# Kernel tuning notes

Measured on AMD Instinct MI355X. Metric: run time of the kernel, lower is better.

Reference implementation:

```python
import jax, jax.numpy as jnp
import numpy as np

B, H, W, C = 2, 128, 128, 256
WS = 8            # current_window (query window)
KW = 16           # halo_window = 2*current_window
HEADS = 8
HD = C // HEADS
PRETRAIN = 8
CPB_HIDDEN = 512


def _rel_bias_consts():
    halo = (KW - WS) // 2
    coords = np.arange(1 - WS - halo, WS + halo, dtype=np.float32)  # length WS+KW-1 = 23
    tab = np.stack(np.meshgrid(coords, coords, indexing='ij'), axis=-1)  # [23,23,2]
    tab = tab * (8.0 / (PRETRAIN - 1.0))
    tab = np.sign(tab) * np.log1p(np.abs(tab)) / np.log(8.0)
    tab = tab.reshape(-1, 2).astype(np.float32)                      # [529,2]
    qi = np.arange(WS)
    qg = np.stack(np.meshgrid(qi, qi, indexing='ij')).reshape(2, -1)  # [2,64]
    ki = np.arange(KW)
    kg = np.stack(np.meshgrid(ki, ki, indexing='ij')).reshape(2, -1)  # [2,256]
    rel = qg[:, :, None] - kg[:, None] + (KW - 1)
    idx = (rel[0] * (WS + KW - 1) + rel[1]).reshape(-1).astype(np.int32)  # [64*256]
    return tab, idx

_REL_TAB, _REL_IDX = _rel_bias_consts()


def setup_inputs() -> dict:
    key = jax.random.key(0)
    ks = jax.random.split(key, 12)
    s = 0.02
    return {
        'x': jax.random.normal(ks[0], (B, H, W, C), jnp.float32),
        'w_qkv': jax.random.normal(ks[1], (C, 3 * C), jnp.float32) * s,
        'w_dw': jax.random.normal(ks[2], (3, 3, 1, 3 * C), jnp.float32) * s,  # depthwise HWIO
        'ln_g': jnp.ones((3 * C,), jnp.float32),
        'ln_b': jnp.zeros((3 * C,), jnp.float32),
        'q_bias': jnp.zeros((C,), jnp.float32),
        'v_bias': jnp.zeros((C,), jnp.float32),
        'logit_scale': jnp.full((HEADS, 1, 1), np.log(10.0), jnp.float32),
        'cpb_w1': jax.random.normal(ks[3], (2, CPB_HIDDEN), jnp.float32) * s,
        'cpb_b1': jnp.zeros((CPB_HIDDEN,), jnp.float32),
        'cpb_w2': jax.random.normal(ks[4], (CPB_HIDDEN, HEADS), jnp.float32) * s,
        'w_proj': jax.random.normal(ks[5], (C, C), jnp.float32) * s,
    }


def _l2n(t):
    # tf.math.l2_normalize with epsilon=1.55e-5
    return t * jax.lax.rsqrt(jnp.maximum(jnp.sum(t * t, -1, keepdims=True), 1.55e-5))


def reference(x, w_qkv, w_dw, ln_g, ln_b, q_bias, v_bias, logit_scale,
              cpb_w1, cpb_b1, cpb_w2, w_proj):
    nWh, nWw = H // WS, W // WS
    nW = nWh * nWw
    # qkv 1x1 conv + depthwise 3x3 + layernorm + (q,0,v) bias
    qkv = jnp.einsum('bhwc,cd->bhwd', x, w_qkv)
    qkv = jax.lax.conv_general_dilated(
        qkv, w_dw, (1, 1), 'SAME',
        dimension_numbers=('NHWC', 'HWIO', 'NHWC'), feature_group_count=3 * C)
    mu = jnp.mean(qkv, -1, keepdims=True)
    var = jnp.var(qkv, -1, keepdims=True)
    qkv = (qkv - mu) * jax.lax.rsqrt(var + 1e-5) * ln_g + ln_b
    qkv = qkv + jnp.concatenate([q_bias, jnp.zeros_like(q_bias), v_bias])
    q, kv = qkv[..., :C], qkv[..., C:]
    # window partition of q: [B*nW, heads, WS*WS, HD]
    qp = q.reshape(B, nWh, WS, nWw, WS, HEADS, HD)
    qp = qp.transpose(0, 1, 3, 5, 2, 4, 6).reshape(B * nW, HEADS, WS * WS, HD)
    # halo partition of kv: overlapping KWxKW patches, stride WS
    halo = (KW - WS) // 2
    kvp = jnp.pad(kv, ((0, 0), (halo, halo), (halo, halo), (0, 0)))
    ridx = (np.arange(nWh) * WS)[:, None] + np.arange(KW)[None]  # [nWh,KW]
    cidx = (np.arange(nWw) * WS)[:, None] + np.arange(KW)[None]  # [nWw,KW]
    kvp = kvp[:, ridx][:, :, :, cidx]               # [B,nWh,KW,nWw,KW,2C]
    kvp = kvp.transpose(0, 1, 3, 2, 4, 5).reshape(B * nW, KW * KW, 2, HEADS, HD)
    k = kvp[:, :, 0].transpose(0, 2, 1, 3)          # [B*nW, heads, KW*KW, HD]
    v = kvp[:, :, 1].transpose(0, 2, 1, 3)
    # cosine attention with clamped learned log-scale
    scale = jnp.exp(jnp.minimum(logit_scale, np.float32(np.log(100.0))))
    attn = jnp.einsum('whqd,whkd->whqk', _l2n(qp) * scale, _l2n(k))
    # continuous relative position bias (CPB MLP + gather)
    hidden = jax.nn.relu(jnp.asarray(_REL_TAB) @ cpb_w1 + cpb_b1)
    bias_tab = jax.nn.sigmoid(hidden @ cpb_w2) * 16.0        # [529, heads]
    rb = bias_tab[_REL_IDX].reshape(WS * WS, KW * KW, HEADS).transpose(2, 0, 1)
    attn = jax.nn.softmax(attn + rb[None], axis=-1)
    out = jnp.einsum('whqk,whkd->whqd', attn, v)             # [B*nW, heads, 64, HD]
    # reverse window partition
    out = out.reshape(B, nWh, nWw, HEADS, WS, WS, HD)
    out = out.transpose(0, 1, 4, 2, 5, 3, 6).reshape(B, H, W, C)
    return jnp.einsum('bhwc,cd->bhwd', out, w_proj)
```

## Files before the change

kernel.cpp:

```cpp
#include <hip/hip_runtime.h>
#include <hip/hip_bf16.h>
#include <hip/hip_fp16.h>
#include <cstddef>
#include <cstdint>

#define BB 2
#define HH 128
#define WW 128
#define CC 256
#define WSZ 8
#define KWIN 16
#define NHEADS 8
#define HD 32
#define C3 768
#define NPIX 32768
#define NWIN 512

typedef short    bf16x8 __attribute__((ext_vector_type(8)));
typedef _Float16 half8  __attribute__((ext_vector_type(8)));
typedef _Float16 half4v __attribute__((ext_vector_type(4)));
typedef float    f32x4  __attribute__((ext_vector_type(4)));

__device__ inline short f2bf(float f) {
    union { float f; unsigned u; } v; v.f = f;
    unsigned r = (v.u + 0x7fffu + ((v.u >> 16) & 1u)) >> 16;
    return (short)r;
}

__device__ inline void gload_lds16(const _Float16* g, _Float16* l) {
    __builtin_amdgcn_global_load_lds(
        (const __attribute__((address_space(1))) unsigned int*)g,
        (__attribute__((address_space(3))) unsigned int*)l, 16, 0, 0);
}

__global__ __launch_bounds__(64) void cpb_kernel(const float* __restrict__ w1,
                                                 const float* __restrict__ b1,
                                                 const float* __restrict__ w2,
                                                 float* __restrict__ btab) {
    const int e = blockIdx.x;
    const int i = e / 23, j = e % 23;
    const float inv_log8 = 1.0f / logf(8.0f);
    float c0 = (float)(i - 11) * (8.0f / 7.0f);
    float c1 = (float)(j - 11) * (8.0f / 7.0f);
    float f0 = copysignf(log1pf(fabsf(c0)) * inv_log8, c0);
    float f1 = copysignf(log1pf(fabsf(c1)) * inv_log8, c1);

    const int t = threadIdx.x;
    float acc[8] = {0.f,0.f,0.f,0.f,0.f,0.f,0.f,0.f};
    for (int kk = 0; kk < 8; kk++) {
        int k = kk * 64 + t;
        float hid = f0 * w1[k] + f1 * w1[512 + k] + b1[k];
        hid = fmaxf(hid, 0.f);
        #pragma unroll
        for (int h = 0; h < 8; h++) acc[h] += hid * w2[k * 8 + h];
    }
    #pragma unroll
    for (int h = 0; h < 8; h++) {
        #pragma unroll
        for (int off = 32; off >= 1; off >>= 1) acc[h] += __shfl_xor(acc[h], off);
    }
    if (t < 8) {
        float v = acc[t];
        btab[e * 8 + t] = 16.0f / (1.0f + expf(-v));
    }
}

__global__ __launch_bounds__(256) void cvt_f32_f16(const float* __restrict__ src,
                                                   _Float16* __restrict__ dst,
                                                   int n4) {
    int i = blockIdx.x * 256 + threadIdx.x;
    if (i >= n4) return;
    float4 v = *(const float4*)(src + (size_t)i * 4);
    half4v o; o[0] = (_Float16)v.x; o[1] = (_Float16)v.y;
    o[2] = (_Float16)v.z; o[3] = (_Float16)v.w;
    *(half4v*)(dst + (size_t)i * 4) = o;
}

__global__ __launch_bounds__(256) void transpose_cvt(const float* __restrict__ src,
                                                     _Float16* __restrict__ dst,
                                                     int R, int Cn) {
    __shared__ float t[32][33];
    const int bx = blockIdx.x, by = blockIdx.y;
    const int tx = threadIdx.x & 31, ty = threadIdx.x >> 5;
    #pragma unroll
    for (int i = 0; i < 4; i++) {
        int r = by * 32 + ty + i * 8;
        t[ty + i * 8][tx] = src[(size_t)r * Cn + bx * 32 + tx];
    }
    __syncthreads();
    #pragma unroll
    for (int i = 0; i < 4; i++) {
        int dr = bx * 32 + ty + i * 8;
        dst[(size_t)dr * R + by * 32 + tx] = (_Float16)t[tx][ty + i * 8];
    }
}

template <typename OT>
__global__ __launch_bounds__(256) void gemm_f16(const _Float16* __restrict__ A,
                                                const _Float16* __restrict__ Bt,
                                                OT* __restrict__ C,
                                                int M, int N, int K) {
    __shared__ _Float16 Ash[128][64];
    __shared__ _Float16 Bsh[128][64];
    const int tid = threadIdx.x;
    const int wv = tid >> 6, ln = tid & 63;
    const int quad = ln >> 4, l15 = ln & 15;
    const int rowb = blockIdx.y * 128;
    const int colb = blockIdx.x * 128;
    const int wm = (wv >> 1) * 64, wn = (wv & 1) * 64;

    const int r8 = ln >> 3, g = ln & 7;
    const int kg = g ^ r8;

    f32x4 acc[4][4] = {};
    for (int k0 = 0; k0 < K; k0 += 64) {
        #pragma unroll
        for (int i = 0; i < 4; i++) {
            const int m = wv * 32 + i * 8 + r8;
            gload_lds16(A + (size_t)(rowb + m) * K + k0 + kg * 8,
                        &Ash[wv * 32 + i * 8][0]);
            gload_lds16(Bt + (size_t)(colb + m) * K + k0 + kg * 8,
                        &Bsh[wv * 32 + i * 8][0]);
        }
        __syncthreads();
        #pragma unroll
        for (int kk = 0; kk < 2; kk++) {
            const int phys = ((kk * 4 + quad) ^ (l15 & 7)) * 8;
            half8 a[4], b[4];
            #pragma unroll
            for (int i = 0; i < 4; i++)
                a[i] = *(const half8*)&Ash[wm + i * 16 + l15][phys];
            #pragma unroll
            for (int j = 0; j < 4; j++)
                b[j] = *(const half8*)&Bsh[wn + j * 16 + l15][phys];
            #pragma unroll
            for (int i = 0; i < 4; i++)
                #pragma unroll
                for (int j = 0; j < 4; j++)
                    acc[i][j] = __builtin_amdgcn_mfma_f32_16x16x32_f16(
                        a[i], b[j], acc[i][j], 0, 0, 0);
        }
        __syncthreads();
    }
    #pragma unroll
    for (int i = 0; i < 4; i++) {
        #pragma unroll
        for (int reg = 0; reg < 4; reg++) {
            const size_t row = rowb + wm + i * 16 + quad * 4 + reg;
            #pragma unroll
            for (int j = 0; j < 4; j++) {
                C[row * N + colb + wn + j * 16 + l15] = (OT)acc[i][j][reg];
            }
        }
    }
}

__global__ __launch_bounds__(256) void dwconv_ln(const _Float16* __restrict__ in,
                                                 const float* __restrict__ wdw,
                                                 const float* __restrict__ g,
                                                 const float* __restrict__ bt,
                                                 const float* __restrict__ qb,
                                                 const float* __restrict__ vb,
                                                 _Float16* __restrict__ out) {
    __shared__ _Float16 S[3 * 10 * C3];
    __shared__ _Float16 Wl[9 * C3];
    __shared__ float sred[4][8][2];

    const int t = threadIdx.x;
    const int pix0 = blockIdx.x * 8;
    const int b = pix0 >> 14, y = (pix0 >> 7) & 127, x0 = pix0 & 127;

    for (int u = t; u < 864; u += 256) {
        const float4 w0 = *(const float4*)(wdw + u * 8);
        const float4 w1 = *(const float4*)(wdw + u * 8 + 4);
        half8 w;
        w[0] = (_Float16)w0.x; w[1] = (_Float16)w0.y;
        w[2] = (_Float16)w0.z; w[3] = (_Float16)w0.w;
        w[4] = (_Float16)w1.x; w[5] = (_Float16)w1.y;
        w[6] = (_Float16)w1.z; w[7] = (_Float16)w1.w;
        *(half8*)&Wl[u * 8] = w;
    }
    for (int u = t; u < 2880; u += 256) {
        const int r = u / 960, rem = u - r * 960;
        const int c = rem / 96, grp = rem - c * 96;
        const int yy = y + r - 1, xx = x0 + c - 1;
        half8 v = (half8)(_Float16)0;
        if ((unsigned)yy < 128u && (unsigned)xx < 128u)
            v = *(const half8*)(in + (((size_t)(b * 128 + yy) * 128 + xx) * C3)
                                + grp * 8);
        *(half8*)&S[u * 8] = v;
    }
    __syncthreads();

    const int p = t & 7, gidx = t >> 3;
    float acc[3][8] = {};
    #pragma unroll
    for (int s = 0; s < 3; s++) {
        const int grp = gidx + s * 32;
        half8 w[9];
        #pragma unroll
        for (int tap = 0; tap < 9; tap++)
            w[tap] = *(const half8*)&Wl[(tap * 96 + grp) * 8];
        #pragma unroll
        for (int r = 0; r < 3; r++) {
            #pragma unroll
            for (int dx = 0; dx < 3; dx++) {
                const half8 v = *(const half8*)&S[((r * 10 + p + dx) * 96 + grp) * 8];
                const half8 wt = w[r * 3 + dx];
                #pragma unroll
                for (int i = 0; i < 8; i++)
                    acc[s][i] += (float)v[i] * (float)wt[i];
            }
        }
    }

    float ls = 0.f, lss = 0.f;
    #pragma unroll
    for (int s = 0; s < 3; s++)
        #pragma unroll
        for (int i = 0; i < 8; i++) { ls += acc[s][i]; lss += acc[s][i] * acc[s][i]; }
    ls  += __shfl_xor(ls, 8);  lss += __shfl_xor(lss, 8);
    ls  += __shfl_xor(ls, 16); lss += __shfl_xor(lss, 16);
    ls  += __shfl_xor(ls, 32); lss += __shfl_xor(lss, 32);
    const int wv = t >> 6, lnid = t & 63;
    if (lnid < 8) { sred[wv][lnid][0] = ls; sred[wv][lnid][1] = lss; }
    __syncthreads();
    const float Ssum  = sred[0][p][0] + sred[1][p][0] + sred[2][p][0] + sred[3][p][0];
    const float SSsum = sred[0][p][1] + sred[1][p][1] + sred[2][p][1] + sred[3][p][1];
    const float mu  = Ssum * (1.0f / 768.0f);
    const float var = SSsum * (1.0f / 768.0f) - mu * mu;
    const float rs  = rsqrtf(var + 1e-5f);

    const size_t obase = (size_t)(pix0 + p) * C3;
    #pragma unroll
    for (int s = 0; s < 3; s++) {
        const int ch = gidx * 8 + s * 256;
        const float4 g0 = *(const float4*)(g + ch);
        const float4 g1 = *(const float4*)(g + ch + 4);
        const float4 b0 = *(const float4*)(bt + ch);
        const float4 b1 = *(const float4*)(bt + ch + 4);
        float gg[8] = {g0.x, g0.y, g0.z, g0.w, g1.x, g1.y, g1.z, g1.w};
        float bb[8] = {b0.x, b0.y, b0.z, b0.w, b1.x, b1.y, b1.z, b1.w};
        if (s == 0) {
            const float4 e0 = *(const float4*)(qb + ch);
            const float4 e1 = *(const float4*)(qb + ch + 4);
            bb[0] += e0.x; bb[1] += e0.y; bb[2] += e0.z; bb[3] += e0.w;
            bb[4] += e1.x; bb[5] += e1.y; bb[6] += e1.z; bb[7] += e1.w;
        } else if (s == 2) {
            const float4 e0 = *(const float4*)(vb + ch - 512);
            const float4 e1 = *(const float4*)(vb + ch - 512 + 4);
            bb[0] += e0.x; bb[1] += e0.y; bb[2] += e0.z; bb[3] += e0.w;
            bb[4] += e1.x; bb[5] += e1.y; bb[6] += e1.z; bb[7] += e1.w;
        }
        half8 o;
        #pragma unroll
        for (int i = 0; i < 8; i++)
            o[i] = (_Float16)((acc[s][i] - mu) * rs * gg[i] + bb[i]);
        *(half8*)(out + obase + ch) = o;
    }
}

__global__ __launch_bounds__(256) void attn_mfma(const _Float16* __restrict__ qkv,
                                                 const float* __restrict__ bias_tab,
                                                 const float* __restrict__ logit_scale,
                                                 _Float16* __restrict__ out) {
    const int blk = blockIdx.x;
    const int h = blk & 7;
    const int wid = blk >> 3;
    const int b = wid >> 8;
    const int wy = (wid >> 4) & 15;
    const int wx = wid & 15;
    const int tid = threadIdx.x;
    const int wave = tid >> 6, lane = tid & 63;
    const int quad = lane >> 4, l15 = lane & 15;

    __shared__ short Kl[256][40];
    __shared__ short Vt[32][264];
    __shared__ short Pl[4][16][256];
    __shared__ float btab[529];

    for (int e = tid; e < 529; e += 256) btab[e] = bias_tab[e * 8 + h];

    {
        const int j = tid;
        const int kr = j >> 4, kcc = j & 15;
        const int gy = wy * 8 - 4 + kr, gx = wx * 8 - 4 + kcc;
        const bool inb = ((unsigned)gy < 128u) && ((unsigned)gx < 128u);
        const _Float16* p = qkv +
            (((size_t)(b * 128 + (inb ? gy : 0)) * 128 + (inb ? gx : 0)) * C3) +
            256 + h * HD;
        float kreg[32];
        float s2 = 0.f;
        #pragma unroll
        for (int d8 = 0; d8 < 32; d8 += 8) {
            half8 kk, vv;
            if (inb) { kk = *(const half8*)(p + d8); vv = *(const half8*)(p + 256 + d8); }
            else     { kk = (half8)(_Float16)0;      vv = (half8)(_Float16)0; }
            #pragma unroll
            for (int u = 0; u < 8; u++) {
                float kf = (float)kk[u];
                kreg[d8 + u] = kf;
                s2 += kf * kf;
                Vt[d8 + u][j] = f2bf((float)vv[u]);
            }
        }
        const float r = rsqrtf(fmaxf(s2, 1.55e-5f));
        #pragma unroll
        for (int d = 0; d < 32; d++) Kl[j][d] = f2bf(kreg[d] * r);
    }
    __syncthreads();

    const float lscale = __expf(fminf(logit_scale[h], 4.60517019f));
    const float Mshift = lscale + 16.0f;
    const int qrow = wave * 16 + l15;
    const int qr = qrow >> 3, qc = qrow & 7;
    const int qy = wy * 8 + qr, qx = wx * 8 + qc;
    bf16x8 afrag;
    {
        const _Float16* qp = qkv + (((size_t)(b * 128 + qy) * 128 + qx) * C3) + h * HD + quad * 8;
        half8 q8 = *(const half8*)qp;
        float qf[8];
        float s2 = 0.f;
        #pragma unroll
        for (int u = 0; u < 8; u++) { qf[u] = (float)q8[u]; s2 += qf[u] * qf[u]; }
        s2 += __shfl_xor(s2, 16);
        s2 += __shfl_xor(s2, 32);
        const float rq = rsqrtf(fmaxf(s2, 1.55e-5f)) * lscale;
        #pragma unroll
        for (int u = 0; u < 8; u++) afrag[u] = f2bf(qf[u] * rq);
    }

    float lsum[4] = {0.f, 0.f, 0.f, 0.f};
    for (int nt = 0; nt < 16; nt++) {
        bf16x8 bfrag = *(const bf16x8*)&Kl[nt * 16 + l15][quad * 8];
        f32x4 s = {0.f, 0.f, 0.f, 0.f};
        s = __builtin_amdgcn_mfma_f32_16x16x32_bf16(afrag, bfrag, s, 0, 0, 0);
        #pragma unroll
        for (int reg = 0; reg < 4; reg++) {
            const int q  = quad * 4 + reg;
            const int gq = wave * 16 + q;
            const int rqr = gq >> 3, rqc = gq & 7;
            const float rb = btab[(rqr - nt + 15) * 23 + (rqc - l15 + 15)];
            const float pv = __expf(s[reg] + rb - Mshift);
            lsum[reg] += pv;
            Pl[wave][q][(nt * 16 + l15) ^ ((q & 12) << 2)] = f2bf(pv);
        }
    }
    #pragma unroll
    for (int reg = 0; reg < 4; reg++) {
        float v = lsum[reg];
        v += __shfl_xor(v, 1); v += __shfl_xor(v, 2);
        v += __shfl_xor(v, 4); v += __shfl_xor(v, 8);
        lsum[reg] = 1.0f / v;
    }

    f32x4 d0 = {0.f, 0.f, 0.f, 0.f};
    f32x4 d1 = {0.f, 0.f, 0.f, 0.f};
    #pragma unroll
    for (int ch = 0; ch < 8; ch++) {
        bf16x8 pa = *(const bf16x8*)&Pl[wave][l15][(ch * 32 + quad * 8) ^ ((l15 & 12) << 2)];
        bf16x8 b0 = *(const bf16x8*)&Vt[l15][ch * 32 + quad * 8];
        bf16x8 b1 = *(const bf16x8*)&Vt[l15 + 16][ch * 32 + quad * 8];
        d0 = __builtin_amdgcn_mfma_f32_16x16x32_bf16(pa, b0, d0, 0, 0, 0);
        d1 = __builtin_amdgcn_mfma_f32_16x16x32_bf16(pa, b1, d1, 0, 0, 0);
    }

    #pragma unroll
    for (int reg = 0; reg < 4; reg++) {
        const int gq = wave * 16 + quad * 4 + reg;
        const int oqr = gq >> 3, oqc = gq & 7;
        const int oy = wy * 8 + oqr, ox = wx * 8 + oqc;
        _Float16* op = out + (((size_t)(b * 128 + oy) * 128 + ox) * CC) + h * HD;
        op[l15]      = (_Float16)(d0[reg] * lsum[reg]);
        op[16 + l15] = (_Float16)(d1[reg] * lsum[reg]);
    }
}

extern "C" void kernel_launch(void* const* d_in, const int* in_sizes, int n_in,
                              void* d_out, int out_size, void* d_ws, size_t ws_size,
                              hipStream_t stream) {
    const float* x           = (const float*)d_in[0];
    const float* w_qkv       = (const float*)d_in[1];
    const float* w_dw        = (const float*)d_in[2];
    const float* ln_g        = (const float*)d_in[3];
    const float* ln_b        = (const float*)d_in[4];
    const float* q_bias      = (const float*)d_in[5];
    const float* v_bias      = (const float*)d_in[6];
    const float* logit_scale = (const float*)d_in[7];
    const float* cpb_w1      = (const float*)d_in[8];
    const float* cpb_b1      = (const float*)d_in[9];
    const float* cpb_w2      = (const float*)d_in[10];
    const float* w_proj      = (const float*)d_in[11];
    float* out = (float*)d_out;

    char* ws = (char*)d_ws;
    _Float16* xh     = (_Float16*)(ws);
    _Float16* qkv0h  = (_Float16*)(ws + 16777216);
    _Float16* qkvh   = (_Float16*)(ws + 67108864);
    _Float16* attnh  = (_Float16*)(ws + 117440512);
    _Float16* wqkvT  = (_Float16*)(ws + 134217728);
    _Float16* wprojT = (_Float16*)(ws + 134610944);
    float*    btab   = (float*)   (ws + 134742016);

    cpb_kernel<<<529, 64, 0, stream>>>(cpb_w1, cpb_b1, cpb_w2, btab);
    cvt_f32_f16<<<(NPIX * CC / 4 + 255) / 256, 256, 0, stream>>>(x, xh, NPIX * CC / 4);
    transpose_cvt<<<dim3(C3 / 32, CC / 32), 256, 0, stream>>>(w_qkv, wqkvT, CC, C3);
    transpose_cvt<<<dim3(CC / 32, CC / 32), 256, 0, stream>>>(w_proj, wprojT, CC, CC);

    gemm_f16<_Float16><<<dim3(C3 / 128, NPIX / 128), 256, 0, stream>>>(
        xh, wqkvT, qkv0h, NPIX, C3, CC);
    dwconv_ln<<<NPIX / 8, 256, 0, stream>>>(qkv0h, w_dw, ln_g, ln_b, q_bias,
                                            v_bias, qkvh);
    attn_mfma<<<NWIN * NHEADS, 256, 0, stream>>>(qkvh, btab, logit_scale, attnh);
    gemm_f16<float><<<dim3(CC / 128, NPIX / 128), 256, 0, stream>>>(
        attnh, wprojT, out, NPIX, CC, CC);
}
```

Baseline: 284.6 us.

## Fuse input f32 conversion into QKV GEMM and restructure dwconv and attention

Drops the separate f32->f16 conversion pass over x: the new QKV GEMM reads the f32 activations and converts them while staging into LDS, which removes a full write and re-read of the activation. The depthwise weights are converted once in a tiny kernel and read from global memory, so the per-block LDS weight staging goes away, and the halo tile in LDS gets an XOR swizzle to cut bank conflicts. The V channel is now written as bf16 so attention can copy it without converting. Attention stores K in an MFMA-fragment layout as f16, folds the max shift into the bias table, and interleaves the PV MFMAs with the score loop in two halves, which halves the P buffer. The changes carry some risk: the A tile is loaded synchronously with no prefetch, and the halo swizzle must index consistently between stores and loads.

```diff
diff --git a/kernel.cpp b/kernel.cpp
--- a/kernel.cpp
+++ b/kernel.cpp
@@ -18,7 +18,6 @@
 
 typedef short    bf16x8 __attribute__((ext_vector_type(8)));
 typedef _Float16 half8  __attribute__((ext_vector_type(8)));
-typedef _Float16 half4v __attribute__((ext_vector_type(4)));
 typedef float    f32x4  __attribute__((ext_vector_type(4)));
 
 __device__ inline short f2bf(float f) {
@@ -65,15 +64,10 @@
     }
 }
 
-__global__ __launch_bounds__(256) void cvt_f32_f16(const float* __restrict__ src,
-                                                   _Float16* __restrict__ dst,
-                                                   int n4) {
+__global__ __launch_bounds__(256) void cvt_wdw(const float* __restrict__ src,
+                                               _Float16* __restrict__ dst) {
     int i = blockIdx.x * 256 + threadIdx.x;
-    if (i >= n4) return;
-    float4 v = *(const float4*)(src + (size_t)i * 4);
-    half4v o; o[0] = (_Float16)v.x; o[1] = (_Float16)v.y;
-    o[2] = (_Float16)v.z; o[3] = (_Float16)v.w;
-    *(half4v*)(dst + (size_t)i * 4) = o;
+    if (i < 9 * C3) dst[i] = (_Float16)src[i];
 }
 
 __global__ __launch_bounds__(256) void transpose_cvt(const float* __restrict__ src,
@@ -155,31 +149,85 @@
     }
 }
 
+__global__ __launch_bounds__(256) void gemm_qkv(const float* __restrict__ A,
+                                                const _Float16* __restrict__ Bt,
+                                                _Float16* __restrict__ C,
+                                                int M, int N, int K) {
+    __shared__ _Float16 Ash[128][64];
+    __shared__ _Float16 Bsh[128][64];
+    const int tid = threadIdx.x;
+    const int wv = tid >> 6, ln = tid & 63;
+    const int quad = ln >> 4, l15 = ln & 15;
+    const int rowb = blockIdx.y * 128;
+    const int colb = blockIdx.x * 128;
+    const int wm = (wv >> 1) * 64, wn = (wv & 1) * 64;
+    const int r8 = ln >> 3, g = ln & 7;
+    const int kg = g ^ r8;
+
+    f32x4 acc[4][4] = {};
+    for (int k0 = 0; k0 < K; k0 += 64) {
+        #pragma unroll
+        for (int i = 0; i < 4; i++) {
+            const int m = wv * 32 + i * 8 + r8;
+            const float* ap = A + (size_t)(rowb + m) * K + k0 + g * 8;
+            const float4 a0 = *(const float4*)ap;
+            const float4 a1 = *(const float4*)(ap + 4);
+            half8 hv;
+            hv[0] = (_Float16)a0.x; hv[1] = (_Float16)a0.y;
+            hv[2] = (_Float16)a0.z; hv[3] = (_Float16)a0.w;
+            hv[4] = (_Float16)a1.x; hv[5] = (_Float16)a1.y;
+            hv[6] = (_Float16)a1.z; hv[7] = (_Float16)a1.w;
+            *(half8*)&Ash[wv * 32 + i * 8 + r8][kg * 8] = hv;
+            gload_lds16(Bt + (size_t)(colb + m) * K + k0 + kg * 8,
+                        &Bsh[wv * 32 + i * 8][0]);
+        }
+        __syncthreads();
+        #pragma unroll
+        for (int kk = 0; kk < 2; kk++) {
+            const int phys = ((kk * 4 + quad) ^ (l15 & 7)) * 8;
+            half8 a[4], b[4];
+            #pragma unroll
+            for (int i = 0; i < 4; i++)
+                a[i] = *(const half8*)&Ash[wm + i * 16 + l15][phys];
+            #pragma unroll
+            for (int j = 0; j < 4; j++)
+                b[j] = *(const half8*)&Bsh[wn + j * 16 + l15][phys];
+            #pragma unroll
+            for (int i = 0; i < 4; i++)
+                #pragma unroll
+                for (int j = 0; j < 4; j++)
+                    acc[i][j] = __builtin_amdgcn_mfma_f32_16x16x32_f16(
+                        a[i], b[j], acc[i][j], 0, 0, 0);
+        }
+        __syncthreads();
+    }
+    #pragma unroll
+    for (int i = 0; i < 4; i++) {
+        #pragma unroll
+        for (int reg = 0; reg < 4; reg++) {
+            const size_t row = rowb + wm + i * 16 + quad * 4 + reg;
+            #pragma unroll
+            for (int j = 0; j < 4; j++) {
+                C[row * N + colb + wn + j * 16 + l15] = (_Float16)acc[i][j][reg];
+            }
+        }
+    }
+}
+
 __global__ __launch_bounds__(256) void dwconv_ln(const _Float16* __restrict__ in,
-                                                 const float* __restrict__ wdw,
+                                                 const _Float16* __restrict__ wdwh,
                                                  const float* __restrict__ g,
                                                  const float* __restrict__ bt,
                                                  const float* __restrict__ qb,
                                                  const float* __restrict__ vb,
                                                  _Float16* __restrict__ out) {
-    __shared__ _Float16 S[3 * 10 * C3];
-    __shared__ _Float16 Wl[9 * C3];
+    __shared__ _Float16 S[2880 * 8];
     __shared__ float sred[4][8][2];
 
     const int t = threadIdx.x;
     const int pix0 = blockIdx.x * 8;
     const int b = pix0 >> 14, y = (pix0 >> 7) & 127, x0 = pix0 & 127;
 
-    for (int u = t; u < 864; u += 256) {
-        const float4 w0 = *(const float4*)(wdw + u * 8);
-        const float4 w1 = *(const float4*)(wdw + u * 8 + 4);
-        half8 w;
-        w[0] = (_Float16)w0.x; w[1] = (_Float16)w0.y;
-        w[2] = (_Float16)w0.z; w[3] = (_Float16)w0.w;
-        w[4] = (_Float16)w1.x; w[5] = (_Float16)w1.y;
-        w[6] = (_Float16)w1.z; w[7] = (_Float16)w1.w;
-        *(half8*)&Wl[u * 8] = w;
-    }
     for (int u = t; u < 2880; u += 256) {
         const int r = u / 960, rem = u - r * 960;
         const int c = rem / 96, grp = rem - c * 96;
@@ -188,7 +236,8 @@
         if ((unsigned)yy < 128u && (unsigned)xx < 128u)
             v = *(const half8*)(in + (((size_t)(b * 128 + yy) * 128 + xx) * C3)
                                 + grp * 8);
-        *(half8*)&S[u * 8] = v;
+        const int phys = (u & ~7) | ((u ^ c) & 7);
+        *(half8*)&S[phys * 8] = v;
     }
     __syncthreads();
 
@@ -200,12 +249,15 @@
         half8 w[9];
         #pragma unroll
         for (int tap = 0; tap < 9; tap++)
-            w[tap] = *(const half8*)&Wl[(tap * 96 + grp) * 8];
+            w[tap] = *(const half8*)(wdwh + (tap * 96 + grp) * 8);
         #pragma unroll
         for (int r = 0; r < 3; r++) {
             #pragma unroll
             for (int dx = 0; dx < 3; dx++) {
-                const half8 v = *(const half8*)&S[((r * 10 + p + dx) * 96 + grp) * 8];
+                const int c = p + dx;
+                const int u = (r * 10 + c) * 96 + grp;
+                const int phys = (u & ~7) | ((u ^ c) & 7);
+                const half8 v = *(const half8*)&S[phys * 8];
                 const half8 wt = w[r * 3 + dx];
                 #pragma unroll
                 for (int i = 0; i < 8; i++)
@@ -252,11 +304,19 @@
             bb[0] += e0.x; bb[1] += e0.y; bb[2] += e0.z; bb[3] += e0.w;
             bb[4] += e1.x; bb[5] += e1.y; bb[6] += e1.z; bb[7] += e1.w;
         }
-        half8 o;
-        #pragma unroll
-        for (int i = 0; i < 8; i++)
-            o[i] = (_Float16)((acc[s][i] - mu) * rs * gg[i] + bb[i]);
-        *(half8*)(out + obase + ch) = o;
+        if (s == 2) {
+            bf16x8 o;
+            #pragma unroll
+            for (int i = 0; i < 8; i++)
+                o[i] = f2bf((acc[s][i] - mu) * rs * gg[i] + bb[i]);
+            *(bf16x8*)((short*)(out + obase + ch)) = o;
+        } else {
+            half8 o;
+            #pragma unroll
+            for (int i = 0; i < 8; i++)
+                o[i] = (_Float16)((acc[s][i] - mu) * rs * gg[i] + bb[i]);
+            *(half8*)(out + obase + ch) = o;
+        }
     }
 }
 
@@ -274,12 +334,14 @@
     const int wave = tid >> 6, lane = tid & 63;
     const int quad = lane >> 4, l15 = lane & 15;
 
-    __shared__ short Kl[256][40];
+    __shared__ _Float16 Bf[16 * 64 * 8];
     __shared__ short Vt[32][264];
-    __shared__ short Pl[4][16][256];
+    __shared__ short Pl[4][16][128];
     __shared__ float btab[529];
 
-    for (int e = tid; e < 529; e += 256) btab[e] = bias_tab[e * 8 + h];
+    const float lscale = __expf(fminf(logit_scale[h], 4.60517019f));
+    const float Mshift = lscale + 16.0f;
+    for (int e = tid; e < 529; e += 256) btab[e] = bias_tab[e * 8 + h] - Mshift;
 
     {
         const int j = tid;
@@ -289,33 +351,39 @@
         const _Float16* p = qkv +
             (((size_t)(b * 128 + (inb ? gy : 0)) * 128 + (inb ? gx : 0)) * C3) +
             256 + h * HD;
+        const short* vp = (const short*)(p + 256);
         float kreg[32];
         float s2 = 0.f;
         #pragma unroll
-        for (int d8 = 0; d8 < 32; d8 += 8) {
-            half8 kk, vv;
-            if (inb) { kk = *(const half8*)(p + d8); vv = *(const half8*)(p + 256 + d8); }
-            else     { kk = (half8)(_Float16)0;      vv = (half8)(_Float16)0; }
+        for (int d8 = 0; d8 < 4; d8++) {
+            half8 kk;
+            bf16x8 vv;
+            if (inb) { kk = *(const half8*)(p + d8 * 8); vv = *(const bf16x8*)(vp + d8 * 8); }
+            else     { kk = (half8)(_Float16)0;          vv = (bf16x8)(short)0; }
             #pragma unroll
             for (int u = 0; u < 8; u++) {
-                float kf = (float)kk[u];
-                kreg[d8 + u] = kf;
+                const float kf = (float)kk[u];
+                kreg[d8 * 8 + u] = kf;
                 s2 += kf * kf;
-                Vt[d8 + u][j] = f2bf((float)vv[u]);
+                Vt[d8 * 8 + u][j] = vv[u];
             }
         }
         const float r = rsqrtf(fmaxf(s2, 1.55e-5f));
         #pragma unroll
-        for (int d = 0; d < 32; d++) Kl[j][d] = f2bf(kreg[d] * r);
+        for (int d8 = 0; d8 < 4; d8++) {
+            half8 hv;
+            #pragma unroll
+            for (int u = 0; u < 8; u++)
+                hv[u] = (_Float16)(kreg[d8 * 8 + u] * r);
+            *(half8*)&Bf[(((j >> 4) * 64) + d8 * 16 + (j & 15)) * 8] = hv;
+        }
     }
     __syncthreads();
 
-    const float lscale = __expf(fminf(logit_scale[h], 4.60517019f));
-    const float Mshift = lscale + 16.0f;
     const int qrow = wave * 16 + l15;
     const int qr = qrow >> 3, qc = qrow & 7;
     const int qy = wy * 8 + qr, qx = wx * 8 + qc;
-    bf16x8 afrag;
+    half8 afrag;
     {
         const _Float16* qp = qkv + (((size_t)(b * 128 + qy) * 128 + qx) * C3) + h * HD + quad * 8;
         half8 q8 = *(const half8*)qp;
@@ -327,23 +395,39 @@
         s2 += __shfl_xor(s2, 32);
         const float rq = rsqrtf(fmaxf(s2, 1.55e-5f)) * lscale;
         #pragma unroll
-        for (int u = 0; u < 8; u++) afrag[u] = f2bf(qf[u] * rq);
+        for (int u = 0; u < 8; u++) afrag[u] = (_Float16)(qf[u] * rq);
     }
 
     float lsum[4] = {0.f, 0.f, 0.f, 0.f};
-    for (int nt = 0; nt < 16; nt++) {
-        bf16x8 bfrag = *(const bf16x8*)&Kl[nt * 16 + l15][quad * 8];
-        f32x4 s = {0.f, 0.f, 0.f, 0.f};
-        s = __builtin_amdgcn_mfma_f32_16x16x32_bf16(afrag, bfrag, s, 0, 0, 0);
-        #pragma unroll
-        for (int reg = 0; reg < 4; reg++) {
-            const int q  = quad * 4 + reg;
-            const int gq = wave * 16 + q;
-            const int rqr = gq >> 3, rqc = gq & 7;
-            const float rb = btab[(rqr - nt + 15) * 23 + (rqc - l15 + 15)];
-            const float pv = __expf(s[reg] + rb - Mshift);
-            lsum[reg] += pv;
-            Pl[wave][q][(nt * 16 + l15) ^ ((q & 12) << 2)] = f2bf(pv);
+    f32x4 d0 = {0.f, 0.f, 0.f, 0.f};
+    f32x4 d1 = {0.f, 0.f, 0.f, 0.f};
+    #pragma unroll
+    for (int hf = 0; hf < 2; hf++) {
+        #pragma unroll
+        for (int ntl = 0; ntl < 8; ntl++) {
+            const int nt = hf * 8 + ntl;
+            half8 bfrag = *(const half8*)&Bf[(nt * 64 + lane) * 8];
+            f32x4 s = {0.f, 0.f, 0.f, 0.f};
+            s = __builtin_amdgcn_mfma_f32_16x16x32_f16(afrag, bfrag, s, 0, 0, 0);
+            #pragma unroll
+            for (int reg = 0; reg < 4; reg++) {
+                const int q  = quad * 4 + reg;
+                const int gq = wave * 16 + q;
+                const int rqr = gq >> 3, rqc = gq & 7;
+                const float rb = btab[(rqr - nt + 15) * 23 + (rqc - l15 + 15)];
+                const float pv = __expf(s[reg] + rb);
+                lsum[reg] += pv;
+                Pl[wave][q][(ntl * 16 + l15) ^ ((q & 12) << 2)] = f2bf(pv);
+            }
+        }
+        #pragma unroll
+        for (int ch = 0; ch < 4; ch++) {
+            const int kb = hf * 128 + ch * 32;
+            bf16x8 pa = *(const bf16x8*)&Pl[wave][l15][(ch * 32 + quad * 8) ^ ((l15 & 12) << 2)];
+            bf16x8 b0 = *(const bf16x8*)&Vt[l15][kb + quad * 8];
+            bf16x8 b1 = *(const bf16x8*)&Vt[l15 + 16][kb + quad * 8];
+            d0 = __builtin_amdgcn_mfma_f32_16x16x32_bf16(pa, b0, d0, 0, 0, 0);
+            d1 = __builtin_amdgcn_mfma_f32_16x16x32_bf16(pa, b1, d1, 0, 0, 0);
         }
     }
     #pragma unroll
@@ -352,17 +436,6 @@
         v += __shfl_xor(v, 1); v += __shfl_xor(v, 2);
         v += __shfl_xor(v, 4); v += __shfl_xor(v, 8);
         lsum[reg] = 1.0f / v;
-    }
-
-    f32x4 d0 = {0.f, 0.f, 0.f, 0.f};
-    f32x4 d1 = {0.f, 0.f, 0.f, 0.f};
-    #pragma unroll
-    for (int ch = 0; ch < 8; ch++) {
-        bf16x8 pa = *(const bf16x8*)&Pl[wave][l15][(ch * 32 + quad * 8) ^ ((l15 & 12) << 2)];
-        bf16x8 b0 = *(const bf16x8*)&Vt[l15][ch * 32 + quad * 8];
-        bf16x8 b1 = *(const bf16x8*)&Vt[l15 + 16][ch * 32 + quad * 8];
-        d0 = __builtin_amdgcn_mfma_f32_16x16x32_bf16(pa, b0, d0, 0, 0, 0);
-        d1 = __builtin_amdgcn_mfma_f32_16x16x32_bf16(pa, b1, d1, 0, 0, 0);
     }
 
     #pragma unroll
@@ -394,22 +467,22 @@
     float* out = (float*)d_out;
 
     char* ws = (char*)d_ws;
-    _Float16* xh     = (_Float16*)(ws);
-    _Float16* qkv0h  = (_Float16*)(ws + 16777216);
-    _Float16* qkvh   = (_Float16*)(ws + 67108864);
-    _Float16* attnh  = (_Float16*)(ws + 117440512);
-    _Float16* wqkvT  = (_Float16*)(ws + 134217728);
-    _Float16* wprojT = (_Float16*)(ws + 134610944);
-    float*    btab   = (float*)   (ws + 134742016);
+    _Float16* qkv0h  = (_Float16*)(ws);
+    _Float16* qkvh   = (_Float16*)(ws + 50331648);
+    _Float16* attnh  = (_Float16*)(ws + 100663296);
+    _Float16* wqkvT  = (_Float16*)(ws + 117440512);
+    _Float16* wprojT = (_Float16*)(ws + 117833728);
+    _Float16* wdwh   = (_Float16*)(ws + 117964800);
+    float*    btab   = (float*)   (ws + 117981184);
 
     cpb_kernel<<<529, 64, 0, stream>>>(cpb_w1, cpb_b1, cpb_w2, btab);
-    cvt_f32_f16<<<(NPIX * CC / 4 + 255) / 256, 256, 0, stream>>>(x, xh, NPIX * CC / 4);
+    cvt_wdw<<<27, 256, 0, stream>>>(w_dw, wdwh);
     transpose_cvt<<<dim3(C3 / 32, CC / 32), 256, 0, stream>>>(w_qkv, wqkvT, CC, C3);
     transpose_cvt<<<dim3(CC / 32, CC / 32), 256, 0, stream>>>(w_proj, wprojT, CC, CC);
 
-    gemm_f16<_Float16><<<dim3(C3 / 128, NPIX / 128), 256, 0, stream>>>(
-        xh, wqkvT, qkv0h, NPIX, C3, CC);
-    dwconv_ln<<<NPIX / 8, 256, 0, stream>>>(qkv0h, w_dw, ln_g, ln_b, q_bias,
+    gemm_qkv<<<dim3(C3 / 128, NPIX / 128), 256, 0, stream>>>(
+        x, wqkvT, qkv0h, NPIX, C3, CC);
+    dwconv_ln<<<NPIX / 8, 256, 0, stream>>>(qkv0h, wdwh, ln_g, ln_b, q_bias,
                                             v_bias, qkvh);
     attn_mfma<<<NWIN * NHEADS, 256, 0, stream>>>(qkvh, btab, logit_scale, attnh);
     gemm_f16<float><<<dim3(CC / 128, NPIX / 128), 256, 0, stream>>>(
```

New measurement: 253.1 us. -11.1%, faster.
